# Optimization experiments

Measured on AMD Instinct MI355X. Metric: run time of the kernel, lower is better.

The kernel has to match this reference:

```python
import jax, jax.numpy as jnp
import numpy as np

H, W, N, B = 64, 64, 512, 32


def setup_inputs() -> dict:
    key = jax.random.key(0)
    k1, _ = jax.random.split(key)
    data = jax.random.normal(k1, (B, N, 8), dtype=jnp.float32)
    opacity = jnp.ones((N, 1), dtype=jnp.float32)
    return {"data": data, "opacity": opacity}


def reference(data, opacity):
    # data: (B, N, 8) -> image (B, 3, H, W)
    xy = jnp.tanh(data[..., :2])                       # (B,N,2) in [-1,1]
    scale = jnp.abs(data[..., 2:4]) + 0.3              # (B,N,2)
    theta = jax.nn.sigmoid(data[..., 4]) * (2.0 * np.pi)  # (B,N)
    color = data[..., 5:8]                             # (B,N,3)

    # NDC -> pixel coords (GaussianImage convention)
    px = 0.5 * ((xy[..., 0] + 1.0) * W - 1.0)          # (B,N)
    py = 0.5 * ((xy[..., 1] + 1.0) * H - 1.0)

    # 2D covariance: R diag(s^2) R^T
    c, s = jnp.cos(theta), jnp.sin(theta)
    s0sq, s1sq = scale[..., 0] ** 2, scale[..., 1] ** 2
    cov_a = c * c * s0sq + s * s * s1sq                # (B,N)
    cov_b = c * s * (s0sq - s1sq)
    cov_c = s * s * s0sq + c * c * s1sq
    det = cov_a * cov_c - cov_b * cov_b
    # conic = inverse covariance
    con_a = cov_c / det
    con_b = -cov_b / det
    con_c = cov_a / det

    xs = jnp.arange(W, dtype=jnp.float32)              # pixel x coords
    ys = jnp.arange(H, dtype=jnp.float32)
    dx = xs[None, None, :] - px[..., None]             # (B,N,W)
    dy = ys[None, None, :] - py[..., None]             # (B,N,H)

    # sigma = 0.5*(A dx^2 + C dy^2) + B dx dy  -> (B,N,H,W)
    sigma = (0.5 * con_a[..., None, None] * (dx[:, :, None, :] ** 2)
             + 0.5 * con_c[..., None, None] * (dy[:, :, :, None] ** 2)
             + con_b[..., None, None] * dy[:, :, :, None] * dx[:, :, None, :])
    alpha = opacity[None, :, 0, None, None] * jnp.exp(-sigma)  # (B,N,H,W)

    # sum blending: out[b,c,h,w] = sum_n alpha[b,n,h,w] * color[b,n,c]
    img = jnp.einsum('bnhw,bnc->bchw', alpha, color)
    return img
```

## Files before the change

### kernel.cpp

```cpp
#include <hip/hip_runtime.h>
#include <math.h>

#define Hh 64
#define Ww 64
#define Nn 512
#define Bb 32
#define NPIX (Hh * Ww)
#define TCUT 16.0f

#define L2E 1.4426950408889634f

__device__ __forceinline__ float fast_sigmoid(float x) {
    float e = __builtin_amdgcn_exp2f(-x * L2E);
    return __builtin_amdgcn_rcpf(1.0f + e);
}
__device__ __forceinline__ float fast_tanh(float x) {
    float e = __builtin_amdgcn_exp2f(x * (-2.0f * L2E));
    return fmaf(2.0f, __builtin_amdgcn_rcpf(1.0f + e), -1.0f);
}

__global__ __launch_bounds__(512, 8) void gs_fused(const float* __restrict__ data,
                                                   const float* __restrict__ opacity,
                                                   float* __restrict__ out) {
    __shared__ float4 sA[Nn];
    __shared__ float4 sB[Nn];
    __shared__ float  sC[Nn];
    __shared__ float4 sD[Nn];
    __shared__ short  slist[8][Nn / 4];
    __shared__ float  comb[2][3][3][64];

    int bid = blockIdx.x;
    int tp  = bid & 31;
    int b   = bid >> 5;
    int t   = threadIdx.x;
    int base = b * Nn;

    {
        int n = t;
        const float4* dp = (const float4*)(data) + (size_t)(base + n) * 2;
        float4 d0 = dp[0];
        float4 d1 = dp[1];

        float xy0 = fast_tanh(d0.x);
        float xy1 = fast_tanh(d0.y);
        float s0 = fabsf(d0.z) + 0.3f;
        float s1 = fabsf(d0.w) + 0.3f;
        float u  = fast_sigmoid(d1.x);
        float c  = __builtin_amdgcn_cosf(u);
        float s  = __builtin_amdgcn_sinf(u);

        float px = 0.5f * ((xy0 + 1.0f) * (float)Ww - 1.0f);
        float py = 0.5f * ((xy1 + 1.0f) * (float)Hh - 1.0f);

        float s0sq = s0 * s0, s1sq = s1 * s1;
        float cov_a = c * c * s0sq + s * s * s1sq;
        float cov_b = c * s * (s0sq - s1sq);
        float cov_c = s * s * s0sq + c * c * s1sq;
        float det = cov_a * cov_c - cov_b * cov_b;
        float inv = __builtin_amdgcn_rcpf(det);
        float con_a = cov_c * inv;
        float con_b = -cov_b * inv;
        float con_c = cov_a * inv;

        float a2 = -0.5f * con_a * L2E;
        float b2 = -con_b * L2E;
        float c2 = -0.5f * con_c * L2E;

        float q1 = -(2.0f * a2 * px + b2 * py);
        float q2 = -(2.0f * c2 * py + b2 * px);
        float q0 = a2 * px * px + b2 * px * py + c2 * py * py;

        float det2 = 4.0f * a2 * c2 - b2 * b2;
        float rinv = __builtin_amdgcn_rcpf(det2);
        float xext = __builtin_amdgcn_sqrtf(fmaxf(4.0f * TCUT * (-c2) * rinv, 0.0f));
        float yext = __builtin_amdgcn_sqrtf(fmaxf(4.0f * TCUT * (-a2) * rinv, 0.0f));

        float op = opacity[n];

        sA[n] = make_float4(q0, q1, q2, a2);
        sB[n] = make_float4(b2, c2, op * d1.y, op * d1.z);
        sC[n] = op * d1.w;
        sD[n] = make_float4(px, py, xext, yext);
    }
    __syncthreads();

    int w        = t >> 6;
    int lane     = t & 63;
    int tile_sel = w >> 2;
    int q        = w & 3;
    int tile     = (tp << 1) | tile_sel;
    int tx0      = (tile & 7) * 8;
    int ty0      = (tile >> 3) * 8;
    float fxq0 = (float)tx0, fxq1 = (float)(tx0 + 7);
    float fyq0 = (float)ty0, fyq1 = (float)(ty0 + 7);

    short* wl = slist[w];
    int cnt = 0;
#pragma unroll
    for (int r = 0; r < 2; ++r) {
        int ln = q * 128 + r * 64 + lane;
        float4 D = sD[ln];
        bool keep = (D.x + D.z >= fxq0) && (D.x - D.z <= fxq1) &&
                    (D.y + D.w >= fyq0) && (D.y - D.w <= fyq1);
        unsigned long long m = __ballot(keep);
        int pos = (int)__popcll(m & ((1ull << lane) - 1ull));
        if (keep) wl[cnt + pos] = (short)ln;
        cnt += (int)__popcll(m);
    }

    float fx = (float)(tx0 + (lane & 7));
    float fy = (float)(ty0 + (lane >> 3));
    float fx2 = fx * fx;
    float fxy = fx * fy;
    float fy2 = fy * fy;

    float accr = 0.0f, accg = 0.0f, accb = 0.0f;
#pragma unroll 4
    for (int i = 0; i < cnt; ++i) {
        int ln = wl[i];
        float4 A  = sA[ln];
        float4 Bv = sB[ln];
        float  ob = sC[ln];
        float sgm = fmaf(A.y, fx, A.x);
        sgm = fmaf(A.z, fy, sgm);
        sgm = fmaf(A.w, fx2, sgm);
        sgm = fmaf(Bv.x, fxy, sgm);
        sgm = fmaf(Bv.y, fy2, sgm);
        float e = __builtin_amdgcn_exp2f(sgm);
        accr = fmaf(e, Bv.z, accr);
        accg = fmaf(e, Bv.w, accg);
        accb = fmaf(e, ob, accb);
    }

    if (q > 0) {
        comb[tile_sel][q - 1][0][lane] = accr;
        comb[tile_sel][q - 1][1][lane] = accg;
        comb[tile_sel][q - 1][2][lane] = accb;
    }
    __syncthreads();
    if (q == 0) {
        accr += comb[tile_sel][0][0][lane] + comb[tile_sel][1][0][lane] + comb[tile_sel][2][0][lane];
        accg += comb[tile_sel][0][1][lane] + comb[tile_sel][1][1][lane] + comb[tile_sel][2][1][lane];
        accb += comb[tile_sel][0][2][lane] + comb[tile_sel][1][2][lane] + comb[tile_sel][2][2][lane];
        int pix = (ty0 + (lane >> 3)) * Ww + tx0 + (lane & 7);
        size_t obase = (size_t)b * 3 * NPIX + (size_t)pix;
        out[obase]            = accr;
        out[obase + NPIX]     = accg;
        out[obase + 2 * NPIX] = accb;
    }
}

extern "C" void kernel_launch(void* const* d_in, const int* in_sizes, int n_in,
                              void* d_out, int out_size, void* d_ws, size_t ws_size,
                              hipStream_t stream) {
    const float* data    = (const float*)d_in[0];
    const float* opacity = (const float*)d_in[1];
    float* out = (float*)d_out;

    gs_fused<<<Bb * 32, 512, 0, stream>>>(data, opacity, out);
}
```

Measured before the change: 10.84 us.

## Balance splat work across warps by pairing tiles and proportional warp assignment

After: 12.23 us. +12.9%, slower.

```diff
diff --git a/kernel.cpp b/kernel.cpp
--- a/kernel.cpp
+++ b/kernel.cpp
@@ -26,8 +26,10 @@
     __shared__ float4 sB[Nn];
     __shared__ float  sC[Nn];
     __shared__ float4 sD[Nn];
-    __shared__ short  slist[8][Nn / 4];
-    __shared__ float  comb[2][3][3][64];
+    __shared__ short  seg[8][128];
+    __shared__ short  tlist[2][Nn];
+    __shared__ int    scnt[8];
+    __shared__ float  comb[6][3][64];
 
     int bid = blockIdx.x;
     int tp  = bid & 31;
@@ -84,17 +86,16 @@
     }
     __syncthreads();
 
-    int w        = t >> 6;
-    int lane     = t & 63;
-    int tile_sel = w >> 2;
-    int q        = w & 3;
-    int tile     = (tp << 1) | tile_sel;
-    int tx0      = (tile & 7) * 8;
-    int ty0      = (tile >> 3) * 8;
-    float fxq0 = (float)tx0, fxq1 = (float)(tx0 + 7);
-    float fyq0 = (float)ty0, fyq1 = (float)(ty0 + 7);
+    int w    = t >> 6;
+    int lane = t & 63;
+    int tsel = w >> 2;
+    int q    = w & 3;
+    int ctile = tsel ? (63 - tp) : tp;
+    int ctx0 = (ctile & 7) * 8;
+    int cty0 = (ctile >> 3) * 8;
 
-    short* wl = slist[w];
+    float fxq0 = (float)ctx0, fxq1 = (float)(ctx0 + 7);
+    float fyq0 = (float)cty0, fyq1 = (float)(cty0 + 7);
     int cnt = 0;
 #pragma unroll
     for (int r = 0; r < 2; ++r) {
@@ -104,9 +105,32 @@
                     (D.y + D.w >= fyq0) && (D.y - D.w <= fyq1);
         unsigned long long m = __ballot(keep);
         int pos = (int)__popcll(m & ((1ull << lane) - 1ull));
-        if (keep) wl[cnt + pos] = (short)ln;
+        if (keep) seg[w][cnt + pos] = (short)ln;
         cnt += (int)__popcll(m);
     }
+    if (lane == 0) scnt[w] = cnt;
+    __syncthreads();
+
+    int c0 = scnt[0] + scnt[1] + scnt[2] + scnt[3];
+    int c1 = scnt[4] + scnt[5] + scnt[6] + scnt[7];
+    int off = 0;
+    for (int j = tsel * 4; j < w; ++j) off += scnt[j];
+    for (int i = lane; i < cnt; i += 64) tlist[tsel][off + i] = seg[w][i];
+    __syncthreads();
+
+    int total = c0 + c1;
+    int n0 = 4;
+    if (total > 0) {
+        n0 = (int)(8.0f * (float)c0 / (float)total + 0.5f);
+        n0 = n0 < 1 ? 1 : (n0 > 7 ? 7 : n0);
+    }
+    int tt, rank, nt;
+    if (w < n0) { tt = 0; rank = w;      nt = n0;     }
+    else        { tt = 1; rank = w - n0; nt = 8 - n0; }
+    int ct    = tt ? c1 : c0;
+    int ttile = tt ? (63 - tp) : tp;
+    int tx0 = (ttile & 7) * 8;
+    int ty0 = (ttile >> 3) * 8;
 
     float fx = (float)(tx0 + (lane & 7));
     float fy = (float)(ty0 + (lane >> 3));
@@ -116,8 +140,8 @@
 
     float accr = 0.0f, accg = 0.0f, accb = 0.0f;
 #pragma unroll 4
-    for (int i = 0; i < cnt; ++i) {
-        int ln = wl[i];
+    for (int idx = rank; idx < ct; idx += nt) {
+        int ln = tlist[tt][idx];
         float4 A  = sA[ln];
         float4 Bv = sB[ln];
         float  ob = sC[ln];
@@ -132,16 +156,21 @@
         accb = fmaf(e, ob, accb);
     }
 
-    if (q > 0) {
-        comb[tile_sel][q - 1][0][lane] = accr;
-        comb[tile_sel][q - 1][1][lane] = accg;
-        comb[tile_sel][q - 1][2][lane] = accb;
+    if (rank > 0) {
+        int slot = tt ? (n0 - 1 + rank - 1) : (rank - 1);
+        comb[slot][0][lane] = accr;
+        comb[slot][1][lane] = accg;
+        comb[slot][2][lane] = accb;
     }
     __syncthreads();
-    if (q == 0) {
-        accr += comb[tile_sel][0][0][lane] + comb[tile_sel][1][0][lane] + comb[tile_sel][2][0][lane];
-        accg += comb[tile_sel][0][1][lane] + comb[tile_sel][1][1][lane] + comb[tile_sel][2][1][lane];
-        accb += comb[tile_sel][0][2][lane] + comb[tile_sel][1][2][lane] + comb[tile_sel][2][2][lane];
+    if (rank == 0) {
+        int s0 = tt ? (n0 - 1) : 0;
+        int ns = (tt ? (8 - n0) : n0) - 1;
+        for (int j = 0; j < ns; ++j) {
+            accr += comb[s0 + j][0][lane];
+            accg += comb[s0 + j][1][lane];
+            accb += comb[s0 + j][2][lane];
+        }
         int pix = (ty0 + (lane >> 3)) * Ww + tx0 + (lane & 7);
         size_t obase = (size_t)b * 3 * NPIX + (size_t)pix;
         out[obase]            = accr;
```
